# Performance work log

Hardware: AMD Instinct MI355X
Metric: run time of the kernel (lower is better)

Reference implementation:

```python
import jax, jax.numpy as jnp
import numpy as np

D_MODEL = 512
D_STATE = 64
D_CONV = 4
D_INNER = 1024   # expand=2 * d_model (mamba_ssm default)
DT_RANK = 32     # ceil(d_model/16)
NUM_CLASSES = 8
B, T, P, F = 8, 250, 20, 24   # x: [B, T*P=5000, F=24]
FLAT = T * P * F              # 120000 = fc1 input dim


def _mamba(u, in_proj_w, conv_w, conv_b, x_proj_w, dt_proj_w, dt_proj_b, A_log, D, out_proj_w):
    # u: [b, L, d_model]
    b, L, _ = u.shape
    xz = jnp.einsum('bld,ed->ble', u, in_proj_w)      # [b, L, 2*d_inner]
    x, z = jnp.split(xz, 2, axis=-1)                  # each [b, L, d_inner]
    # depthwise causal conv1d, kernel width D_CONV, truncated to L
    x_pad = jnp.pad(x, ((0, 0), (D_CONV - 1, 0), (0, 0)))
    x = sum(x_pad[:, k:k + L, :] * conv_w[:, k] for k in range(D_CONV)) + conv_b
    x = jax.nn.silu(x)
    x_dbl = jnp.einsum('bld,ed->ble', x, x_proj_w)    # [b, L, dt_rank + 2*d_state]
    dt, Bm, Cm = jnp.split(x_dbl, [DT_RANK, DT_RANK + D_STATE], axis=-1)
    dt = jax.nn.softplus(jnp.einsum('blr,dr->bld', dt, dt_proj_w) + dt_proj_b)  # [b, L, d_inner]
    A = -jnp.exp(A_log)                               # [d_inner, d_state]

    def step(h, inp):
        dt_t, B_t, C_t, u_t = inp                     # [b,d_in], [b,d_st], [b,d_st], [b,d_in]
        dA = jnp.exp(dt_t[:, :, None] * A)            # [b, d_in, d_st]
        dBu = dt_t[:, :, None] * B_t[:, None, :] * u_t[:, :, None]
        h = h * dA + dBu
        y = jnp.einsum('bds,bs->bd', h, C_t)
        return h, y

    xs = (jnp.swapaxes(dt, 0, 1), jnp.swapaxes(Bm, 0, 1), jnp.swapaxes(Cm, 0, 1), jnp.swapaxes(x, 0, 1))
    h0 = jnp.zeros((b, D_INNER, D_STATE), dtype=u.dtype)
    _, ys = jax.lax.scan(step, h0, xs)                # ys: [L, b, d_inner]
    y = jnp.swapaxes(ys, 0, 1) + x * D
    y = y * jax.nn.silu(z)
    return jnp.einsum('bld,ed->ble', y, out_proj_w)   # [b, L, d_model]


def setup_inputs() -> dict:
    key = jax.random.key(0)
    ks = jax.random.split(key, 16)
    n = lambda k, shape, s=0.02: jax.random.normal(k, shape, jnp.float32) * s
    return {
        'x': jax.random.normal(ks[0], (B, T * P, F), jnp.float32),
        'in_proj_w': n(ks[1], (2 * D_INNER, D_MODEL)),
        'conv_w': n(ks[2], (D_INNER, D_CONV), 0.1),
        'conv_b': jnp.zeros((D_INNER,), jnp.float32),
        'x_proj_w': n(ks[3], (DT_RANK + 2 * D_STATE, D_INNER)),
        'dt_proj_w': n(ks[4], (D_INNER, DT_RANK), 0.1),
        'dt_proj_b': jnp.full((D_INNER,), -4.6, jnp.float32),  # softplus -> dt ~ 0.01
        'A_log': jnp.log(jnp.broadcast_to(jnp.arange(1, D_STATE + 1, dtype=jnp.float32), (D_INNER, D_STATE))),
        'D': jnp.ones((D_INNER,), jnp.float32),
        'out_proj_w': n(ks[5], (D_MODEL, D_INNER)),
        'fc1_w': n(ks[6], (512, FLAT), 0.003),
        'fc1_b': jnp.zeros((512,), jnp.float32),
        'fc2_w': n(ks[7], (256, 512)),
        'fc2_b': jnp.zeros((256,), jnp.float32),
        'fc3_w': n(ks[8], (64, 256)),
        'fc3_b': jnp.zeros((64,), jnp.float32),
        'fc4_w': n(ks[9], (NUM_CLASSES, 64)),
        'fc4_b': jnp.zeros((NUM_CLASSES,), jnp.float32),
    }


def reference(x, in_proj_w, conv_w, conv_b, x_proj_w, dt_proj_w, dt_proj_b, A_log, D, out_proj_w,
              fc1_w, fc1_b, fc2_w, fc2_b, fc3_w, fc3_b, fc4_w, fc4_b):
    b = x.shape[0]
    u = x.reshape(b, T, P * F)                                   # [b,250,480]
    u = jnp.pad(u, ((0, 0), (0, 0), (0, D_MODEL - P * F)))       # pad 480 -> 512
    y = _mamba(u, in_proj_w, conv_w, conv_b, x_proj_w, dt_proj_w, dt_proj_b, A_log, D, out_proj_w)
    y = jax.nn.selu(y)                                           # AlphaDropout: identity in eval
    y = y[..., :P * F].reshape(b, T * P, F)                      # [b,5000,24]
    y = jnp.swapaxes(y, 1, 2).reshape(b, -1)                     # [b, 24*5000]
    y = y @ fc1_w.T + fc1_b
    y = y @ fc2_w.T + fc2_b
    y = y @ fc3_w.T + fc3_b
    return y @ fc4_w.T + fc4_b
```

## Files before the change

kernel.cpp:

```cpp
#include <hip/hip_runtime.h>
#include <math.h>

#define T_ 250
#define BL 2000
#define KIN 480
#define NFLAT 120000

__device__ __forceinline__ float sigmoidf_(float x){ return 1.0f/(1.0f+expf(-x)); }
__device__ __forceinline__ float siluf_(float x){ return x*sigmoidf_(x); }
__device__ __forceinline__ float softplusf_(float x){ return (x > 20.0f) ? x : log1pf(expf(x)); }
__device__ __forceinline__ float seluf_(float x){
  const float sc = 1.0507009873554804934193349852946f;
  const float al = 1.6732632423543772848170429916717f;
  return x > 0.0f ? sc*x : sc*al*expm1f(x);
}

template<int CTRL>
__device__ __forceinline__ float dpp_add(float x) {
  int t = __builtin_amdgcn_update_dpp(0, __builtin_bit_cast(int, x), CTRL, 0xF, 0xF, true);
  return x + __builtin_bit_cast(float, t);
}

template<int BM, int BN, int BK, int TM, int TN>
__global__ __launch_bounds__(256, 2) void gemm_nt(
    const float* __restrict__ A, const float* __restrict__ W,
    float* __restrict__ C, const float* __restrict__ bias,
    int M, int N, int K, int lda, int ldb, int ldc, int epi)
{
  static_assert(BK == 32, "BK must be 32");
  __shared__ __align__(16) float As[BK][BM + 4];
  __shared__ __align__(16) float Bs[BK][BN + 4];
  constexpr int TNX = BN / TN;
  constexpr int TMX = BM / TM;
  static_assert(TNX * TMX == 256, "256 threads required");
  constexpr int AF4 = BM * BK / 1024;
  constexpr int BF4 = BN * BK / 1024;

  const int tid = threadIdx.x;
  const int tx = tid % TNX;
  const int ty = tid / TNX;
  const int m0 = blockIdx.y * BM;
  const int n0 = blockIdx.x * BN;
  const int kchunk = K / (int)gridDim.z;
  const int k_begin = blockIdx.z * kchunk;
  const int k_end = k_begin + kchunk;

  float acc[TM][TN];
#pragma unroll
  for (int i = 0; i < TM; ++i)
#pragma unroll
    for (int j = 0; j < TN; ++j) acc[i][j] = 0.0f;

  for (int k0 = k_begin; k0 < k_end; k0 += BK) {
#pragma unroll
    for (int i = 0; i < AF4; ++i) {
      int fi = tid + 256 * i;
      int r = fi >> 3;
      int kc = (fi & 7) * 4;
      int m = m0 + r;
      float4 v = make_float4(0.f, 0.f, 0.f, 0.f);
      if (m < M) v = *(const float4*)(A + (size_t)m * lda + k0 + kc);
      As[kc + 0][r] = v.x; As[kc + 1][r] = v.y; As[kc + 2][r] = v.z; As[kc + 3][r] = v.w;
    }
#pragma unroll
    for (int i = 0; i < BF4; ++i) {
      int fi = tid + 256 * i;
      int r = fi >> 3;
      int kc = (fi & 7) * 4;
      int n = n0 + r;
      float4 v = make_float4(0.f, 0.f, 0.f, 0.f);
      if (n < N) v = *(const float4*)(W + (size_t)n * ldb + k0 + kc);
      Bs[kc + 0][r] = v.x; Bs[kc + 1][r] = v.y; Bs[kc + 2][r] = v.z; Bs[kc + 3][r] = v.w;
    }
    __syncthreads();
#pragma unroll
    for (int kk = 0; kk < BK; ++kk) {
      float a[TM], bb[TN];
      if constexpr ((TM & 3) == 0) {
#pragma unroll
        for (int t = 0; t < TM / 4; ++t) {
          float4 v = *(const float4*)&As[kk][ty * TM + t * 4];
          a[t*4+0] = v.x; a[t*4+1] = v.y; a[t*4+2] = v.z; a[t*4+3] = v.w;
        }
      } else {
#pragma unroll
        for (int i = 0; i < TM; ++i) a[i] = As[kk][ty * TM + i];
      }
      if constexpr ((TN & 3) == 0) {
#pragma unroll
        for (int t = 0; t < TN / 4; ++t) {
          float4 v = *(const float4*)&Bs[kk][tx * TN + t * 4];
          bb[t*4+0] = v.x; bb[t*4+1] = v.y; bb[t*4+2] = v.z; bb[t*4+3] = v.w;
        }
      } else {
#pragma unroll
        for (int j = 0; j < TN; ++j) bb[j] = Bs[kk][tx * TN + j];
      }
#pragma unroll
      for (int i = 0; i < TM; ++i)
#pragma unroll
        for (int j = 0; j < TN; ++j) acc[i][j] = fmaf(a[i], bb[j], acc[i][j]);
    }
    __syncthreads();
  }

#pragma unroll
  for (int i = 0; i < TM; ++i) {
    int m = m0 + ty * TM + i;
    if (m >= M) continue;
    if constexpr ((TN & 3) == 0) {
#pragma unroll
      for (int j0 = 0; j0 < TN; j0 += 4) {
        int n = n0 + tx * TN + j0;
        float v[4];
#pragma unroll
        for (int t = 0; t < 4; ++t) {
          float xv = acc[i][j0 + t];
          if (epi == 1) xv = softplusf_(xv + bias[n + t]);
          else if (epi == 2) xv = seluf_(xv);
          v[t] = xv;
        }
        if (epi == 3) {
#pragma unroll
          for (int t = 0; t < 4; ++t)
            if (n + t < N) atomicAdd(&C[(size_t)m * ldc + n + t], v[t]);
        } else if (n + 3 < N) {
          *(float4*)&C[(size_t)m * ldc + n] = make_float4(v[0], v[1], v[2], v[3]);
        } else {
#pragma unroll
          for (int t = 0; t < 4; ++t)
            if (n + t < N) C[(size_t)m * ldc + n + t] = v[t];
        }
      }
    } else {
#pragma unroll
      for (int j = 0; j < TN; ++j) {
        int n = n0 + tx * TN + j;
        if (n >= N) continue;
        float v = acc[i][j];
        if (epi == 1) v = softplusf_(v + bias[n]);
        else if (epi == 2) v = seluf_(v);
        if (epi == 3) atomicAdd(&C[(size_t)m * ldc + n], v);
        else C[(size_t)m * ldc + n] = v;
      }
    }
  }
}

__global__ __launch_bounds__(256) void conv_silu(
    float* __restrict__ xz, const float* __restrict__ cw,
    const float* __restrict__ cb, float* __restrict__ xc)
{
  int id = blockIdx.x * 256 + threadIdx.x;
  if (id >= BL * 1024) return;
  int bl = id >> 10;
  int d = id & 1023;
  int l = bl % T_;
  float4 w4 = *(const float4*)(cw + d * 4);
  float s = cb[d];
  if (l >= 3) s = fmaf(xz[(size_t)(bl - 3) * 2048 + d], w4.x, s);
  if (l >= 2) s = fmaf(xz[(size_t)(bl - 2) * 2048 + d], w4.y, s);
  if (l >= 1) s = fmaf(xz[(size_t)(bl - 1) * 2048 + d], w4.z, s);
  s = fmaf(xz[(size_t)bl * 2048 + d], w4.w, s);
  xc[id] = siluf_(s);
  float z = xz[(size_t)bl * 2048 + 1024 + d];
  xz[(size_t)bl * 2048 + 1024 + d] = siluf_(z);
}

__global__ __launch_bounds__(256) void scan_kernel(
    const float* __restrict__ dtb, const float* __restrict__ xc,
    const float* __restrict__ xdbl, float* __restrict__ xz,
    const float* __restrict__ A_log, const float* __restrict__ Dp)
{
  int tid = threadIdx.x;
  int wv = tid >> 6, lane = tid & 63;
  int c = lane >> 5;
  int u = lane & 31;
  int w = blockIdx.x * 4 + wv;
  int b = w >> 9;
  int d = ((w & 511) << 1) + c;
  const float LOG2E = 1.4426950408889634f;
  float2 al = *(const float2*)(A_log + (size_t)d * 64 + u * 2);
  float am0 = -expf(al.x) * LOG2E;
  float am1 = -expf(al.y) * LOG2E;
  float Dv = Dp[d];
  float h0 = 0.f, h1 = 0.f;
  const float* dtp = dtb + (size_t)b * 256000 + d;
  const float* xp  = xc  + (size_t)b * 256000 + d;
  const float* zp  = xz  + (size_t)b * 512000 + 1024 + d;
  float*       yp  = xz  + (size_t)b * 512000 + d;
  const float* bp  = xdbl + (size_t)b * 40000 + 32 + u * 2;
  const float* cp  = bp + 64;

  float dt_f[2], xv_f[2], sz_f[2];
  float2 B_f[2], C_f[2];
#pragma unroll
  for (int i = 0; i < 2; ++i) {
    dt_f[i] = dtp[i * 1024];
    xv_f[i] = xp[i * 1024];
    sz_f[i] = zp[i * 2048];
    B_f[i] = *(const float2*)(bp + i * 160);
    C_f[i] = *(const float2*)(cp + i * 160);
  }
  const bool outlane = (u == 16);

#pragma unroll 2
  for (int l = 0; l < T_; ++l) {
    int slot = l & 1;
    float dt = dt_f[slot], xv = xv_f[slot], sz = sz_f[slot];
    float2 Bv = B_f[slot], Cv = C_f[slot];
    dt_f[slot] = dtp[(size_t)(l + 2) * 1024];
    xv_f[slot] = xp[(size_t)(l + 2) * 1024];
    sz_f[slot] = zp[(size_t)(l + 2) * 2048];
    B_f[slot]  = *(const float2*)(bp + (size_t)(l + 2) * 160);
    C_f[slot]  = *(const float2*)(cp + (size_t)(l + 2) * 160);

    float dtx = dt * xv;
    h0 = fmaf(h0, exp2f(dt * am0), dtx * Bv.x);
    h1 = fmaf(h1, exp2f(dt * am1), dtx * Bv.y);
    float p = fmaf(h1, Cv.y, h0 * Cv.x);
    p = dpp_add<0xB1>(p);
    p = dpp_add<0x4E>(p);
    p = dpp_add<0x124>(p);
    p = dpp_add<0x128>(p);
    p = dpp_add<0x142>(p);
    if (outlane) yp[(size_t)l * 2048] = fmaf(xv, Dv, p) * sz;
  }
}

__global__ __launch_bounds__(256) void transpose_k(
    const float* __restrict__ ym, float* __restrict__ yfl)
{
  int id = blockIdx.x * 256 + threadIdx.x;
  if (id >= 8 * NFLAT) return;
  int b = id / NFLAT;
  int r = id % NFLAT;
  int f = r / 5000;
  int qq = r % 5000;
  int tt = qq / 20;
  int p = qq % 20;
  yfl[id] = ym[(size_t)(b * T_ + tt) * KIN + p * 24 + f];
}

__global__ __launch_bounds__(256) void fc1_kernel(
    const float* __restrict__ yfl, const float* __restrict__ W,
    float* __restrict__ r1)
{
  int blk = blockIdx.x;
  int ks = blk % 24;
  int cg = blk / 24;
  int wv = threadIdx.x >> 6;
  int lane = threadIdx.x & 63;
  int c0 = cg * 16 + wv * 4;
  const float* W0 = W + (size_t)c0 * NFLAT;
  float acc[4][8];
#pragma unroll
  for (int cc = 0; cc < 4; ++cc)
#pragma unroll
    for (int b = 0; b < 8; ++b) acc[cc][b] = 0.0f;

  int kbase = ks * 5000;
  int kend = kbase + 5000;
  for (int k = kbase + lane * 4; k + 4 <= kend; k += 256) {
    float4 w0 = *(const float4*)(W0 + k);
    float4 w1 = *(const float4*)(W0 + NFLAT + k);
    float4 w2 = *(const float4*)(W0 + 2 * (size_t)NFLAT + k);
    float4 w3 = *(const float4*)(W0 + 3 * (size_t)NFLAT + k);
#pragma unroll
    for (int b = 0; b < 8; ++b) {
      float4 y = *(const float4*)(yfl + (size_t)b * NFLAT + k);
      acc[0][b] = fmaf(w0.x, y.x, fmaf(w0.y, y.y, fmaf(w0.z, y.z, fmaf(w0.w, y.w, acc[0][b]))));
      acc[1][b] = fmaf(w1.x, y.x, fmaf(w1.y, y.y, fmaf(w1.z, y.z, fmaf(w1.w, y.w, acc[1][b]))));
      acc[2][b] = fmaf(w2.x, y.x, fmaf(w2.y, y.y, fmaf(w2.z, y.z, fmaf(w2.w, y.w, acc[2][b]))));
      acc[3][b] = fmaf(w3.x, y.x, fmaf(w3.y, y.y, fmaf(w3.z, y.z, fmaf(w3.w, y.w, acc[3][b]))));
    }
  }
#pragma unroll
  for (int cc = 0; cc < 4; ++cc)
#pragma unroll
    for (int b = 0; b < 8; ++b) {
      float s = acc[cc][b];
      s += __shfl_xor(s, 1);
      s += __shfl_xor(s, 2);
      s += __shfl_xor(s, 4);
      s += __shfl_xor(s, 8);
      s += __shfl_xor(s, 16);
      s += __shfl_xor(s, 32);
      if (lane == 0) atomicAdd(&r1[b * 512 + c0 + cc], s);
    }
}

__global__ __launch_bounds__(256) void fc2_kernel(
    const float* __restrict__ r1, const float* __restrict__ b1,
    const float* __restrict__ W2, const float* __restrict__ b2,
    float* __restrict__ r2)
{
  int wid = blockIdx.x * 4 + (threadIdx.x >> 6);
  int lane = threadIdx.x & 63;
  int b = wid >> 8;
  int j = wid & 255;
  int off = lane * 8;
  float4 ya = *(const float4*)(r1 + b * 512 + off);
  float4 yb = *(const float4*)(r1 + b * 512 + off + 4);
  float4 ba = *(const float4*)(b1 + off);
  float4 bbv = *(const float4*)(b1 + off + 4);
  float4 wa = *(const float4*)(W2 + (size_t)j * 512 + off);
  float4 wb = *(const float4*)(W2 + (size_t)j * 512 + off + 4);
  float p = (ya.x + ba.x) * wa.x + (ya.y + ba.y) * wa.y +
            (ya.z + ba.z) * wa.z + (ya.w + ba.w) * wa.w +
            (yb.x + bbv.x) * wb.x + (yb.y + bbv.y) * wb.y +
            (yb.z + bbv.z) * wb.z + (yb.w + bbv.w) * wb.w;
  p += __shfl_xor(p, 1);
  p += __shfl_xor(p, 2);
  p += __shfl_xor(p, 4);
  p += __shfl_xor(p, 8);
  p += __shfl_xor(p, 16);
  p += __shfl_xor(p, 32);
  if (lane == 0) r2[b * 256 + j] = p + b2[j];
}

__global__ __launch_bounds__(256) void fc34_kernel(
    const float* __restrict__ r2, const float* __restrict__ W3,
    const float* __restrict__ b3, const float* __restrict__ W4,
    const float* __restrict__ b4, float* __restrict__ out)
{
  __shared__ float a3[512];
  int tid = threadIdx.x;
  for (int o = tid; o < 512; o += 256) {
    int b = o >> 6, j = o & 63;
    float s = b3[j];
    const float* rr = r2 + b * 256;
    const float* wr = W3 + j * 256;
    for (int c = 0; c < 256; c += 4) {
      float4 rv = *(const float4*)(rr + c);
      float4 wv = *(const float4*)(wr + c);
      s = fmaf(rv.x, wv.x, fmaf(rv.y, wv.y, fmaf(rv.z, wv.z, fmaf(rv.w, wv.w, s))));
    }
    a3[o] = s;
  }
  __syncthreads();
  if (tid < 64) {
    int b = tid >> 3, j = tid & 7;
    float s = b4[j];
    const float* ar = a3 + b * 64;
    const float* wr = W4 + j * 64;
    for (int c = 0; c < 64; ++c) s = fmaf(ar[c], wr[c], s);
    out[b * 8 + j] = s;
  }
}

extern "C" void kernel_launch(void* const* d_in, const int* in_sizes, int n_in,
                              void* d_out, int out_size, void* d_ws, size_t ws_size,
                              hipStream_t stream) {
  const float* x      = (const float*)d_in[0];
  const float* w_in   = (const float*)d_in[1];
  const float* conv_w = (const float*)d_in[2];
  const float* conv_b = (const float*)d_in[3];
  const float* w_xp   = (const float*)d_in[4];
  const float* w_dt   = (const float*)d_in[5];
  const float* b_dt   = (const float*)d_in[6];
  const float* A_log  = (const float*)d_in[7];
  const float* Dp     = (const float*)d_in[8];
  const float* w_out  = (const float*)d_in[9];
  const float* w1 = (const float*)d_in[10];
  const float* b1 = (const float*)d_in[11];
  const float* w2 = (const float*)d_in[12];
  const float* b2 = (const float*)d_in[13];
  const float* w3 = (const float*)d_in[14];
  const float* b3 = (const float*)d_in[15];
  const float* w4 = (const float*)d_in[16];
  const float* b4 = (const float*)d_in[17];
  float* out = (float*)d_out;

  float* ws   = (float*)d_ws;
  float* xz   = ws;
  float* xc   = xz + 4096000;
  float* dtb  = xc + 2048000;
  float* ym   = dtb + 2048000;
  float* yfl  = ym + 960000;
  float* xdbl = yfl + 960000;
  float* r1   = xdbl + 320000;
  float* r2   = r1 + 4096;

  hipMemsetAsync(xdbl, 0, (320000 + 4096) * sizeof(float), stream);

  gemm_nt<64, 128, 32, 4, 8><<<dim3(2048 / 128, (BL + 63) / 64, 1), 256, 0, stream>>>(
      x, w_in, xz, nullptr, BL, 2048, KIN, KIN, 512, 2048, 0);

  conv_silu<<<(BL * 1024) / 256, 256, 0, stream>>>(xz, conv_w, conv_b, xc);

  gemm_nt<32, 64, 32, 1, 8><<<dim3(3, (BL + 31) / 32, 2), 256, 0, stream>>>(
      xc, w_xp, xdbl, nullptr, BL, 160, 1024, 1024, 1024, 160, 3);

  gemm_nt<32, 64, 32, 1, 8><<<dim3(1024 / 64, (BL + 31) / 32, 1), 256, 0, stream>>>(
      xdbl, w_dt, dtb, b_dt, BL, 1024, 32, 160, 32, 1024, 1);

  scan_kernel<<<1024, 256, 0, stream>>>(dtb, xc, xdbl, xz, A_log, Dp);

  gemm_nt<64, 64, 32, 4, 4><<<dim3((KIN + 63) / 64, (BL + 63) / 64, 1), 256, 0, stream>>>(
      xz, w_out, ym, nullptr, BL, KIN, 1024, 2048, 1024, KIN, 2);

  transpose_k<<<(8 * NFLAT) / 256, 256, 0, stream>>>(ym, yfl);

  fc1_kernel<<<768, 256, 0, stream>>>(yfl, w1, r1);

  fc2_kernel<<<512, 256, 0, stream>>>(r1, b1, w2, b2, r2);

  fc34_kernel<<<1, 256, 0, stream>>>(r2, w3, b3, w4, b4, out);
}
```

Measured before the change: 754.2 us.

## Fuse transpose into out_proj GEMM epilogue, add register prefetch and deeper scan prefetch

Adds an epilogue mode to the out_proj GEMM that applies SELU and writes directly in the flattened transposed layout fc1 expects, removing the separate transpose kernel and its round trip through memory. The GEMM now prefetches the next K tile into registers while computing the current one. The scan kernel deepens its software prefetch from 2 to 4 steps, running extra guarded iterations. The scattered epilogue writes are uncoalesced, and the scan reads slightly further past each batch's buffer.

```diff
diff --git a/kernel.cpp b/kernel.cpp
--- a/kernel.cpp
+++ b/kernel.cpp
@@ -45,22 +45,17 @@
   const int k_begin = blockIdx.z * kchunk;
   const int k_end = k_begin + kchunk;
 
-  float acc[TM][TN];
-#pragma unroll
-  for (int i = 0; i < TM; ++i)
-#pragma unroll
-    for (int j = 0; j < TN; ++j) acc[i][j] = 0.0f;
-
-  for (int k0 = k_begin; k0 < k_end; k0 += BK) {
+  float4 pa[AF4], pb[BF4];
+
+  auto fetch = [&](int k0) {
 #pragma unroll
     for (int i = 0; i < AF4; ++i) {
       int fi = tid + 256 * i;
       int r = fi >> 3;
       int kc = (fi & 7) * 4;
       int m = m0 + r;
-      float4 v = make_float4(0.f, 0.f, 0.f, 0.f);
-      if (m < M) v = *(const float4*)(A + (size_t)m * lda + k0 + kc);
-      As[kc + 0][r] = v.x; As[kc + 1][r] = v.y; As[kc + 2][r] = v.z; As[kc + 3][r] = v.w;
+      pa[i] = (m < M) ? *(const float4*)(A + (size_t)m * lda + k0 + kc)
+                      : make_float4(0.f, 0.f, 0.f, 0.f);
     }
 #pragma unroll
     for (int i = 0; i < BF4; ++i) {
@@ -68,11 +63,38 @@
       int r = fi >> 3;
       int kc = (fi & 7) * 4;
       int n = n0 + r;
-      float4 v = make_float4(0.f, 0.f, 0.f, 0.f);
-      if (n < N) v = *(const float4*)(W + (size_t)n * ldb + k0 + kc);
-      Bs[kc + 0][r] = v.x; Bs[kc + 1][r] = v.y; Bs[kc + 2][r] = v.z; Bs[kc + 3][r] = v.w;
+      pb[i] = (n < N) ? *(const float4*)(W + (size_t)n * ldb + k0 + kc)
+                      : make_float4(0.f, 0.f, 0.f, 0.f);
+    }
+  };
+
+  fetch(k_begin);
+
+  float acc[TM][TN];
+#pragma unroll
+  for (int i = 0; i < TM; ++i)
+#pragma unroll
+    for (int j = 0; j < TN; ++j) acc[i][j] = 0.0f;
+
+  for (int k0 = k_begin; k0 < k_end; k0 += BK) {
+#pragma unroll
+    for (int i = 0; i < AF4; ++i) {
+      int fi = tid + 256 * i;
+      int r = fi >> 3;
+      int kc = (fi & 7) * 4;
+      As[kc + 0][r] = pa[i].x; As[kc + 1][r] = pa[i].y;
+      As[kc + 2][r] = pa[i].z; As[kc + 3][r] = pa[i].w;
+    }
+#pragma unroll
+    for (int i = 0; i < BF4; ++i) {
+      int fi = tid + 256 * i;
+      int r = fi >> 3;
+      int kc = (fi & 7) * 4;
+      Bs[kc + 0][r] = pb[i].x; Bs[kc + 1][r] = pb[i].y;
+      Bs[kc + 2][r] = pb[i].z; Bs[kc + 3][r] = pb[i].w;
     }
     __syncthreads();
+    if (k0 + BK < k_end) fetch(k0 + BK);
 #pragma unroll
     for (int kk = 0; kk < BK; ++kk) {
       float a[TM], bb[TN];
@@ -102,6 +124,25 @@
         for (int j = 0; j < TN; ++j) acc[i][j] = fmaf(a[i], bb[j], acc[i][j]);
     }
     __syncthreads();
+  }
+
+  if (epi == 4) {
+#pragma unroll
+    for (int i = 0; i < TM; ++i) {
+      int m = m0 + ty * TM + i;
+      if (m >= M) continue;
+      int b = m / 250;
+      int tt = m - b * 250;
+#pragma unroll
+      for (int j = 0; j < TN; ++j) {
+        int n = n0 + tx * TN + j;
+        if (n >= N) continue;
+        int p = n / 24;
+        int f = n - p * 24;
+        C[(size_t)b * NFLAT + (size_t)f * 5000 + tt * 20 + p] = seluf_(acc[i][j]);
+      }
+    }
+    return;
   }
 
 #pragma unroll
@@ -192,28 +233,28 @@
   const float* bp  = xdbl + (size_t)b * 40000 + 32 + u * 2;
   const float* cp  = bp + 64;
 
-  float dt_f[2], xv_f[2], sz_f[2];
-  float2 B_f[2], C_f[2];
-#pragma unroll
-  for (int i = 0; i < 2; ++i) {
-    dt_f[i] = dtp[i * 1024];
-    xv_f[i] = xp[i * 1024];
-    sz_f[i] = zp[i * 2048];
-    B_f[i] = *(const float2*)(bp + i * 160);
-    C_f[i] = *(const float2*)(cp + i * 160);
+  float dt_f[4], xv_f[4], sz_f[4];
+  float2 B_f[4], C_f[4];
+#pragma unroll
+  for (int i = 0; i < 4; ++i) {
+    dt_f[i] = dtp[(size_t)i * 1024];
+    xv_f[i] = xp[(size_t)i * 1024];
+    sz_f[i] = zp[(size_t)i * 2048];
+    B_f[i] = *(const float2*)(bp + (size_t)i * 160);
+    C_f[i] = *(const float2*)(cp + (size_t)i * 160);
   }
   const bool outlane = (u == 16);
 
-#pragma unroll 2
-  for (int l = 0; l < T_; ++l) {
-    int slot = l & 1;
+#pragma unroll 4
+  for (int l = 0; l < 252; ++l) {
+    int slot = l & 3;
     float dt = dt_f[slot], xv = xv_f[slot], sz = sz_f[slot];
     float2 Bv = B_f[slot], Cv = C_f[slot];
-    dt_f[slot] = dtp[(size_t)(l + 2) * 1024];
-    xv_f[slot] = xp[(size_t)(l + 2) * 1024];
-    sz_f[slot] = zp[(size_t)(l + 2) * 2048];
-    B_f[slot]  = *(const float2*)(bp + (size_t)(l + 2) * 160);
-    C_f[slot]  = *(const float2*)(cp + (size_t)(l + 2) * 160);
+    dt_f[slot] = dtp[(size_t)(l + 4) * 1024];
+    xv_f[slot] = xp[(size_t)(l + 4) * 1024];
+    sz_f[slot] = zp[(size_t)(l + 4) * 2048];
+    B_f[slot]  = *(const float2*)(bp + (size_t)(l + 4) * 160);
+    C_f[slot]  = *(const float2*)(cp + (size_t)(l + 4) * 160);
 
     float dtx = dt * xv;
     h0 = fmaf(h0, exp2f(dt * am0), dtx * Bv.x);
@@ -224,22 +265,8 @@
     p = dpp_add<0x124>(p);
     p = dpp_add<0x128>(p);
     p = dpp_add<0x142>(p);
-    if (outlane) yp[(size_t)l * 2048] = fmaf(xv, Dv, p) * sz;
-  }
-}
-
-__global__ __launch_bounds__(256) void transpose_k(
-    const float* __restrict__ ym, float* __restrict__ yfl)
-{
-  int id = blockIdx.x * 256 + threadIdx.x;
-  if (id >= 8 * NFLAT) return;
-  int b = id / NFLAT;
-  int r = id % NFLAT;
-  int f = r / 5000;
-  int qq = r % 5000;
-  int tt = qq / 20;
-  int p = qq % 20;
-  yfl[id] = ym[(size_t)(b * T_ + tt) * KIN + p * 24 + f];
+    if (outlane && l < T_) yp[(size_t)l * 2048] = fmaf(xv, Dv, p) * sz;
+  }
 }
 
 __global__ __launch_bounds__(256) void fc1_kernel(
@@ -381,6 +408,7 @@
   float* xdbl = yfl + 960000;
   float* r1   = xdbl + 320000;
   float* r2   = r1 + 4096;
+  (void)ym;
 
   hipMemsetAsync(xdbl, 0, (320000 + 4096) * sizeof(float), stream);
 
@@ -398,9 +426,7 @@
   scan_kernel<<<1024, 256, 0, stream>>>(dtb, xc, xdbl, xz, A_log, Dp);
 
   gemm_nt<64, 64, 32, 4, 4><<<dim3((KIN + 63) / 64, (BL + 63) / 64, 1), 256, 0, stream>>>(
-      xz, w_out, ym, nullptr, BL, KIN, 1024, 2048, 1024, KIN, 2);
-
-  transpose_k<<<(8 * NFLAT) / 256, 256, 0, stream>>>(ym, yfl);
+      xz, w_out, yfl, nullptr, BL, KIN, 1024, 2048, 1024, KIN, 4);
 
   fc1_kernel<<<768, 256, 0, stream>>>(yfl, w1, r1);
 
```

After: 686.5 us. 9.0% less time.
